# Kernel tuning notes

Measured on AMD Instinct MI355X. Metric: run time of the kernel, lower is better.

## Reference

```python
import jax, jax.numpy as jnp
import numpy as np

B, S, HID, NH = 1, 2048, 2048, 16
HD = HID // NH
HALF = HD // 2
# quantization scales (registered buffers / pack() scales in the original module)
ATTN_IN_SCALE = 0.02   # attn_input_scale: dequant scale of int8 hidden_states
Q_OUT_SCALE = 0.05     # q_output_scale
K_OUT_SCALE = 0.05     # k_output_scale
V_OUT_SCALE = 0.04     # v_output_scale
Q_ROT_SCALE = 0.06     # q_rotary_output_scale
K_ROT_SCALE = 0.06     # k_rotary_output_scale
OUT_IN_SCALE = 0.03    # out_input_scale
W_ALPHA = 0.002        # folded int8 GEMM alpha for q/k/v W8A8B8O8Linear
BETA = 1.0             # bias scale of W8A8B8O8Linear
O_ALPHA = 0.001        # folded alpha for o_proj W8A8BFP32OFP32Linear
PROB_SCALE = 1.0 / 127.0  # attention-prob int8 quant scale
INV_SQRT_HD = float(1.0 / np.sqrt(HD))


def _q8(x):
    # saturating int8 quantization (values kept in float32)
    return jnp.clip(jnp.round(x), -127.0, 127.0)


def setup_inputs() -> dict:
    key = jax.random.key(0)
    ks = jax.random.split(key, 10)
    hidden_states = jax.random.normal(ks[0], (B, S, HID), jnp.float32)
    pos = jnp.arange(S, dtype=jnp.float32)
    inv_freq = 1.0 / (10000.0 ** (jnp.arange(0, HD, 2, dtype=jnp.float32) / HD))
    freqs = pos[:, None] * inv_freq[None, :]          # (S, HD//2)
    cos, sin = jnp.cos(freqs), jnp.sin(freqs)
    w8 = lambda k: jax.random.randint(k, (HID, HID), -127, 128).astype(jnp.float32)
    b8 = lambda k: jax.random.randint(k, (HID,), -127, 128).astype(jnp.float32)
    return dict(
        hidden_states=hidden_states, cos=cos, sin=sin,
        wq=w8(ks[1]), wk=w8(ks[2]), wv=w8(ks[3]), wo=w8(ks[4]),
        bq=b8(ks[5]), bk=b8(ks[6]), bv=b8(ks[7]),
        bo=jax.random.normal(ks[8], (HID,), jnp.float32) * 0.01,
    )


def reference(hidden_states, cos, sin, wq, wk, wv, wo, bq, bk, bv, bo):
    # quantize activations to int8 (done upstream of the module in smoothquant)
    x8 = _q8(hidden_states / ATTN_IN_SCALE)                       # (B,S,HID) int8 vals

    # W8A8B8O8Linear: int8 GEMM, alpha-scaled, int8 bias, saturate to int8
    def lin8(x, w, b):
        return _q8(jnp.einsum('bsi,oi->bso', x, w) * W_ALPHA + BETA * b)

    q8, k8, v8 = lin8(x8, wq, bq), lin8(x8, wk, bk), lin8(x8, wv, bv)

    # int8_rotary_embedding_fwd: dequant -> split-half rotary -> requant
    def rope(x8_flat, in_scale, out_scale):
        x = x8_flat.reshape(B, S, NH, HD) * in_scale
        x0, x1 = x[..., :HALF], x[..., HALF:]
        c, s_ = cos[None, :, None, :], sin[None, :, None, :]
        rot = jnp.concatenate([x0 * c - x1 * s_, x0 * s_ + x1 * c], axis=-1)
        return _q8(rot / out_scale)

    q = rope(q8, Q_OUT_SCALE, Q_ROT_SCALE)                        # (B,S,NH,HD)
    k = rope(k8, K_OUT_SCALE, K_ROT_SCALE)
    v = v8.reshape(B, S, NH, HD)

    # smooth_llama_context_attn_fwd: int8 QK^T -> fp32 scores -> causal softmax
    scores = jnp.einsum('bqhd,bkhd->bhqk', q, k) * (Q_ROT_SCALE * K_ROT_SCALE * INV_SQRT_HD)
    causal = jnp.tril(jnp.ones((S, S), bool))
    scores = jnp.where(causal[None, None], scores, -1e9)
    p = jax.nn.softmax(scores, axis=-1)
    p8 = _q8(p * 127.0)                                           # quantize probs to int8
    # int8 PV bmm, rescale and saturate to int8 for o_proj input
    o8 = _q8(jnp.einsum('bhqk,bkhd->bqhd', p8, v) * (PROB_SCALE * V_OUT_SCALE / OUT_IN_SCALE))
    o8 = o8.reshape(B, S, HID)

    # W8A8BFP32OFP32Linear: int8 GEMM, fp32 alpha + fp32 bias
    out = jnp.einsum('bso,po->bsp', o8, wo) * O_ALPHA + bo
    return out
```

## Files before the change

kernel.cpp:

```cpp
#include <hip/hip_runtime.h>
#include <math.h>

typedef __attribute__((ext_vector_type(4))) int i32x4;
typedef signed char s8;

constexpr int S   = 2048;
constexpr int HID = 2048;
constexpr int NH  = 16;
constexpr int HD  = 128;
constexpr int HALF = 64;

#define SCORE_SCALE ((float)(0.06 * 0.06 * 0.08838834764831845))
#define OSCALE      ((float)(((1.0 / 127.0) * 0.04) / 0.03))

__device__ __forceinline__ float clip127(float r){
  return fminf(fmaxf(r, -127.0f), 127.0f);
}
__device__ __forceinline__ i32x4 mfma_i8(i32x4 a, i32x4 b, i32x4 c){
  return __builtin_amdgcn_mfma_i32_16x16x64_i8(a, b, c, 0, 0, 0);
}
__device__ __forceinline__ void async16(const void* g, void* l){
  __builtin_amdgcn_global_load_lds(
      (const __attribute__((address_space(1))) unsigned*)g,
      (__attribute__((address_space(3))) unsigned*)l, 16, 0, 0);
}
template<int ROWS>
__device__ __forceinline__ void stage_async_swz(s8* dst, const s8* src, int stride){
  const int tid = threadIdx.x;
#pragma unroll
  for (int i = 0; i < ROWS/32; ++i){
    int o = i*256 + tid;
    int row = o >> 3, ch = o & 7;
    async16(src + (size_t)row*stride + ((ch ^ (row & 7))*16), dst + o*16);
  }
}
__device__ __forceinline__ i32x4 rd16(const s8* buf, int row, int ch){
  return *(const i32x4*)(buf + row*128 + ((ch ^ (row & 7))*16));
}
__device__ __forceinline__ int tri_qt(int t){
  int qt = (int)((sqrtf(8.f*t + 1.f) - 1.f)*0.5f);
  while ((qt+1)*(qt+2)/2 <= t) ++qt;
  while (qt*(qt+1)/2 > t) --qt;
  return qt;
}

__global__ void cvt_all(const float* __restrict__ hid, const float* __restrict__ wq,
                        const float* __restrict__ wk, const float* __restrict__ wv,
                        const float* __restrict__ wo, s8* __restrict__ xd,
                        s8* __restrict__ qd, s8* __restrict__ kd,
                        s8* __restrict__ vd, s8* __restrict__ od, int n){
  const float* srcs[5] = {hid, wq, wk, wv, wo};
  s8* dsts[5] = {xd, qd, kd, vd, od};
  int which = blockIdx.y;
  const float* src = srcs[which];
  s8* dst = dsts[which];
  int i = (blockIdx.x * blockDim.x + threadIdx.x) * 4;
  if (i >= n) return;
  float4 v = *(const float4*)(src + i);
  float x[4] = {v.x, v.y, v.z, v.w};
  unsigned packed = 0;
#pragma unroll
  for (int j = 0; j < 4; ++j){
    int b;
    if (which == 0) b = (int)clip127(rintf(x[j] / 0.02f));
    else            b = (int)x[j];
    packed |= ((unsigned)(b & 255)) << (8*j);
  }
  *(unsigned*)(dst + i) = packed;
}

__global__ __launch_bounds__(256)
void gemm_qkv(const s8* __restrict__ A, const s8* __restrict__ W,
              const float* __restrict__ bq, const float* __restrict__ bk,
              const float* __restrict__ bv, s8* __restrict__ Out){
#pragma clang fp contract(off)
  constexpr int Kd = 2048, N = 2048;
  const int z = blockIdx.z;
  const s8* Bt = W + (size_t)z*(4u<<20);
  s8* Y = Out + (size_t)z*(4u<<20);
  const float* bss[3] = {bq, bk, bv};
  const float* bias = bss[z];
  __shared__ __attribute__((aligned(16))) s8 As[128*128];
  __shared__ __attribute__((aligned(16))) s8 Bs[128*128];
  const int lin = blockIdx.x + (blockIdx.y << 4);
  const int virt = (lin & 7)*32 + (lin >> 3);
  const int bm = virt & 15, bn = virt >> 4;
  const int tid = threadIdx.x;
  const int wid = tid >> 6, lane = tid & 63;
  const int wm = wid >> 1, wn = wid & 1;
  const int col16 = lane & 15, g = lane >> 4;
  i32x4 acc[4][4] = {};
  const s8* Ab = A + (size_t)(bm*128)*Kd;
  const s8* Bb = Bt + (size_t)(bn*128)*Kd;
  for (int kt = 0; kt < 16; ++kt){
    stage_async_swz<128>(As, Ab + kt*128, Kd);
    stage_async_swz<128>(Bs, Bb + kt*128, Kd);
    __syncthreads();
#pragma unroll
    for (int kk = 0; kk < 2; ++kk){
      i32x4 af[4], bf[4];
#pragma unroll
      for (int i = 0; i < 4; ++i) af[i] = rd16(As, wm*64 + i*16 + col16, kk*4 + g);
#pragma unroll
      for (int j = 0; j < 4; ++j) bf[j] = rd16(Bs, wn*64 + j*16 + col16, kk*4 + g);
#pragma unroll
      for (int i = 0; i < 4; ++i)
#pragma unroll
        for (int j = 0; j < 4; ++j)
          acc[i][j] = mfma_i8(af[i], bf[j], acc[i][j]);
    }
    __syncthreads();
  }
#pragma unroll
  for (int i = 0; i < 4; ++i){
#pragma unroll
    for (int j = 0; j < 4; ++j){
      int row0 = bm*128 + wm*64 + i*16 + g*4;
      int col  = bn*128 + wn*64 + j*16 + col16;
#pragma unroll
      for (int r = 0; r < 4; ++r){
        float t = (float)acc[i][j][r] * 0.002f;
        t = t + bias[col];
        Y[(size_t)(row0 + r)*N + col] = (s8)(int)clip127(rintf(t));
      }
    }
  }
}

__global__ __launch_bounds__(256)
void gemm_o(const s8* __restrict__ A, const s8* __restrict__ Bt,
            const float* __restrict__ bias, float* __restrict__ Y){
#pragma clang fp contract(off)
  constexpr int Kd = 2048, N = 2048;
  __shared__ __attribute__((aligned(16))) s8 As[128*128];
  __shared__ __attribute__((aligned(16))) s8 Bs[64*128];
  const int lin = blockIdx.x + (blockIdx.y << 4);
  const int virt = (lin & 7)*64 + (lin >> 3);
  const int bm = virt & 15, bn = virt >> 4;
  const int tid = threadIdx.x;
  const int wid = tid >> 6, lane = tid & 63;
  const int wm = wid >> 1, wn = wid & 1;
  const int col16 = lane & 15, g = lane >> 4;
  i32x4 acc[4][2] = {};
  const s8* Ab = A + (size_t)(bm*128)*Kd;
  const s8* Bb = Bt + (size_t)(bn*64)*Kd;
  for (int kt = 0; kt < 16; ++kt){
    stage_async_swz<128>(As, Ab + kt*128, Kd);
    stage_async_swz<64>(Bs, Bb + kt*128, Kd);
    __syncthreads();
#pragma unroll
    for (int kk = 0; kk < 2; ++kk){
      i32x4 af[4], bf[2];
#pragma unroll
      for (int i = 0; i < 4; ++i) af[i] = rd16(As, wm*64 + i*16 + col16, kk*4 + g);
#pragma unroll
      for (int j = 0; j < 2; ++j) bf[j] = rd16(Bs, wn*32 + j*16 + col16, kk*4 + g);
#pragma unroll
      for (int i = 0; i < 4; ++i)
#pragma unroll
        for (int j = 0; j < 2; ++j)
          acc[i][j] = mfma_i8(af[i], bf[j], acc[i][j]);
    }
    __syncthreads();
  }
#pragma unroll
  for (int i = 0; i < 4; ++i){
#pragma unroll
    for (int j = 0; j < 2; ++j){
      int row0 = bm*128 + wm*64 + i*16 + g*4;
      int col  = bn*64 + wn*32 + j*16 + col16;
#pragma unroll
      for (int r = 0; r < 4; ++r){
        float t = (float)acc[i][j][r] * 0.001f;
        t = t + bias[col];
        Y[(size_t)(row0 + r)*N + col] = t;
      }
    }
  }
}

__global__ void rope_qk(s8* __restrict__ q, s8* __restrict__ k,
                        const float* __restrict__ cosp, const float* __restrict__ sinp){
#pragma clang fp contract(off)
  int idx = blockIdx.x * blockDim.x + threadIdx.x;
  int t4 = (idx & 15) * 4;
  int h  = (idx >> 4) & (NH-1);
  int s  = idx >> 8;
  if (s >= S) return;
  float4 c4 = *(const float4*)(cosp + s*HALF + t4);
  float4 s4 = *(const float4*)(sinp + s*HALF + t4);
  float cc[4] = {c4.x, c4.y, c4.z, c4.w}, ss[4] = {s4.x, s4.y, s4.z, s4.w};
  int base = s*HID + h*HD + t4;
  {
    int a0 = *(const int*)(q + base), a1 = *(const int*)(q + base + HALF);
    unsigned o0 = 0, o1 = 0;
#pragma unroll
    for (int j = 0; j < 4; ++j){
      float x0 = (float)((s8)(a0 >> (8*j))) * 0.05f;
      float x1 = (float)((s8)(a1 >> (8*j))) * 0.05f;
      float r0 = x0*cc[j] - x1*ss[j];
      float r1 = x0*ss[j] + x1*cc[j];
      o0 |= ((unsigned)(((int)clip127(rintf(r0 / 0.06f))) & 255)) << (8*j);
      o1 |= ((unsigned)(((int)clip127(rintf(r1 / 0.06f))) & 255)) << (8*j);
    }
    *(unsigned*)(q + base) = o0; *(unsigned*)(q + base + HALF) = o1;
  }
  {
    int a0 = *(const int*)(k + base), a1 = *(const int*)(k + base + HALF);
    unsigned o0 = 0, o1 = 0;
#pragma unroll
    for (int j = 0; j < 4; ++j){
      float x0 = (float)((s8)(a0 >> (8*j))) * 0.05f;
      float x1 = (float)((s8)(a1 >> (8*j))) * 0.05f;
      float r0 = x0*cc[j] - x1*ss[j];
      float r1 = x0*ss[j] + x1*cc[j];
      o0 |= ((unsigned)(((int)clip127(rintf(r0 / 0.06f))) & 255)) << (8*j);
      o1 |= ((unsigned)(((int)clip127(rintf(r1 / 0.06f))) & 255)) << (8*j);
    }
    *(unsigned*)(k + base) = o0; *(unsigned*)(k + base + HALF) = o1;
  }
}

__global__ void vtrans(const s8* __restrict__ v, s8* __restrict__ vt){
  __shared__ __attribute__((aligned(16))) s8 t[128*144];
  int s0 = blockIdx.x * 128, h = blockIdx.y;
  int tid = threadIdx.x;
#pragma unroll
  for (int i = 0; i < 4; ++i){
    int vv = i*256 + tid, r = vv >> 3, ch = vv & 7;
    *(i32x4*)(t + r*144 + ch*16) = *(const i32x4*)(v + (size_t)(s0 + r)*HID + h*HD + ch*16);
  }
  __syncthreads();
#pragma unroll
  for (int i = 0; i < 4; ++i){
    int vv = i*256 + tid, d = vv >> 3, sc = (vv & 7)*16;
    s8 tmp[16];
#pragma unroll
    for (int j = 0; j < 16; ++j) tmp[j] = t[(sc + j)*144 + d];
    *(i32x4*)(vt + (size_t)(h*HD + d)*S + s0 + sc) = *(i32x4*)tmp;
  }
}

__global__ __launch_bounds__(256)
void attn_stats(const s8* __restrict__ qr, const s8* __restrict__ kr,
                float2* __restrict__ stats){
  const int x = blockIdx.x, h = blockIdx.y;
  const int tri = x >> 1, half = x & 1;
  const int qt = tri_qt(tri);
  const int kt = tri - qt*(qt+1)/2;
  const int q0 = qt*128 + half*64;
  const int tid = threadIdx.x, wid = tid >> 6, lane = tid & 63;
  const int col16 = lane & 15, g = lane >> 4;
  __shared__ __attribute__((aligned(16))) s8 Ks[128*128];

  stage_async_swz<128>(Ks, kr + (size_t)(kt*128)*HID + h*HD, HID);
  const s8* qb = qr + (size_t)(q0 + wid*16 + col16)*HID + h*HD + g*16;
  i32x4 aq[2];
  aq[0] = *(const i32x4*)(qb);
  aq[1] = *(const i32x4*)(qb + 64);
  __syncthreads();

  i32x4 sc[8] = {};
#pragma unroll
  for (int kk = 0; kk < 2; ++kk){
#pragma unroll
    for (int j = 0; j < 8; ++j){
      i32x4 bk = rd16(Ks, j*16 + col16, kk*4 + g);
      sc[j] = mfma_i8(aq[kk], bk, sc[j]);
    }
  }

  const bool diag = (kt == qt);
#pragma unroll
  for (int r = 0; r < 4; ++r){
    int rit = half*64 + wid*16 + g*4 + r;
    int qrow = qt*128 + rit;
    int mi = (int)0x80000000;
#pragma unroll
    for (int j = 0; j < 8; ++j){
      int v = sc[j][r];
      if (diag && (kt*128 + j*16 + col16 > qrow)) v = (int)0x80000000;
      mi = max(mi, v);
    }
    mi = max(mi, __shfl_xor(mi, 1));
    mi = max(mi, __shfl_xor(mi, 2));
    mi = max(mi, __shfl_xor(mi, 4));
    mi = max(mi, __shfl_xor(mi, 8));
    float mf = (float)mi * SCORE_SCALE;
    float st = 0.f;
#pragma unroll
    for (int j = 0; j < 8; ++j){
      float arg;
      if (diag && (kt*128 + j*16 + col16 > qrow)) arg = -1e30f;
      else arg = (float)sc[j][r] * SCORE_SCALE - mf;
      st += __expf(arg);
    }
    st += __shfl_xor(st, 1);
    st += __shfl_xor(st, 2);
    st += __shfl_xor(st, 4);
    st += __shfl_xor(st, 8);
    if (col16 == 0) stats[(size_t)(h*136 + tri)*128 + rit] = make_float2(mf, st);
  }
}

__global__ void attn_reduce(const float2* __restrict__ stats, float2* __restrict__ ml){
  const int row = threadIdx.x, qt = blockIdx.x, h = blockIdx.y;
  const int tri = qt*(qt+1)/2;
  float m = -3.0e38f;
  for (int kt = 0; kt <= qt; ++kt)
    m = fmaxf(m, stats[(size_t)(h*136 + tri + kt)*128 + row].x);
  float l = 0.f;
  for (int kt = 0; kt <= qt; ++kt){
    float2 s = stats[(size_t)(h*136 + tri + kt)*128 + row];
    l += s.y * __expf(s.x - m);
  }
  ml[(h*16 + qt)*128 + row] = make_float2(m, l);
}

__global__ __launch_bounds__(256)
void attn_score(const s8* __restrict__ qr, const s8* __restrict__ kr,
                const float2* __restrict__ ml, s8* __restrict__ P8){
  const int x = blockIdx.x, h = blockIdx.y;
  const int tri = x >> 1, half = x & 1;
  const int qt = tri_qt(tri);
  const int kt = tri - qt*(qt+1)/2;
  const int q0 = qt*128 + half*64;
  const int tid = threadIdx.x, wid = tid >> 6, lane = tid & 63;
  const int col16 = lane & 15, g = lane >> 4;
  __shared__ __attribute__((aligned(16))) s8 Ks[128*128];
  __shared__ __attribute__((aligned(16))) s8 Pl[64*128];

  stage_async_swz<128>(Ks, kr + (size_t)(kt*128)*HID + h*HD, HID);
  const s8* qb = qr + (size_t)(q0 + wid*16 + col16)*HID + h*HD + g*16;
  i32x4 aq[2];
  aq[0] = *(const i32x4*)(qb);
  aq[1] = *(const i32x4*)(qb + 64);
  float m[4], c[4];
#pragma unroll
  for (int r = 0; r < 4; ++r){
    float2 t = ml[(h*16 + qt)*128 + half*64 + wid*16 + g*4 + r];
    m[r] = t.x;
    c[r] = 127.0f / t.y;
  }
  __syncthreads();

  const bool diag = (kt == qt);
#pragma unroll
  for (int j = 0; j < 8; ++j){
    i32x4 s0 = {};
    s0 = mfma_i8(aq[0], rd16(Ks, j*16 + col16, g), s0);
    s0 = mfma_i8(aq[1], rd16(Ks, j*16 + col16, 4 + g), s0);
    int colk = j*16 + col16;
#pragma unroll
    for (int r = 0; r < 4; ++r){
      int row = wid*16 + g*4 + r;
      int qrow = q0 + row;
      float p8v = 0.0f;
      if (!diag || (kt*128 + colk) <= qrow){
        float sv = (float)s0[r] * SCORE_SCALE;
        p8v = clip127(rintf(__expf(sv - m[r]) * c[r]));
      }
      Pl[row*128 + colk] = (s8)(int)p8v;
    }
  }
  __syncthreads();
  s8* dst = P8 + (size_t)(h*136 + tri)*16384 + half*8192;
#pragma unroll
  for (int i = 0; i < 2; ++i){
    int o = i*256 + tid;
    *(i32x4*)(dst + o*16) = *(const i32x4*)(Pl + o*16);
  }
}

__global__ __launch_bounds__(256)
void attn_pv(const s8* __restrict__ P8, const s8* __restrict__ vt8,
             s8* __restrict__ o8){
  const int qt = 15 - blockIdx.x;
  const int h = blockIdx.y, dh = blockIdx.z;
  const int tri = qt*(qt+1)/2;
  const int tid = threadIdx.x, wid = tid >> 6, lane = tid & 63;
  const int wm = wid >> 1, wn = wid & 1;
  const int col16 = lane & 15, g = lane >> 4;
  __shared__ __attribute__((aligned(16))) s8 Ps[128*128];
  __shared__ __attribute__((aligned(16))) s8 Vs[64*128];

  i32x4 acc[4][2] = {};
  for (int kt = 0; kt <= qt; ++kt){
    stage_async_swz<128>(Ps, P8 + (size_t)(h*136 + tri + kt)*16384, 128);
    stage_async_swz<64>(Vs, vt8 + (size_t)(h*HD + dh*64)*S + kt*128, S);
    __syncthreads();
#pragma unroll
    for (int kk = 0; kk < 2; ++kk){
      i32x4 af[4], bf[2];
#pragma unroll
      for (int i = 0; i < 4; ++i) af[i] = rd16(Ps, wm*64 + i*16 + col16, kk*4 + g);
#pragma unroll
      for (int j = 0; j < 2; ++j) bf[j] = rd16(Vs, wn*32 + j*16 + col16, kk*4 + g);
#pragma unroll
      for (int i = 0; i < 4; ++i)
#pragma unroll
        for (int j = 0; j < 2; ++j)
          acc[i][j] = mfma_i8(af[i], bf[j], acc[i][j]);
    }
    __syncthreads();
  }
#pragma unroll
  for (int i = 0; i < 4; ++i)
#pragma unroll
    for (int j = 0; j < 2; ++j)
#pragma unroll
      for (int r = 0; r < 4; ++r){
        int row = qt*128 + wm*64 + i*16 + g*4 + r;
        int d = dh*64 + wn*32 + j*16 + col16;
        o8[(size_t)row*HID + h*HD + d] = (s8)(int)clip127(rintf((float)acc[i][j][r] * OSCALE));
      }
}

extern "C" void kernel_launch(void* const* d_in, const int* in_sizes, int n_in,
                              void* d_out, int out_size, void* d_ws, size_t ws_size,
                              hipStream_t stream) {
  const float* hidden = (const float*)d_in[0];
  const float* cosp   = (const float*)d_in[1];
  const float* sinp   = (const float*)d_in[2];
  const float* wq     = (const float*)d_in[3];
  const float* wk     = (const float*)d_in[4];
  const float* wv     = (const float*)d_in[5];
  const float* wo     = (const float*)d_in[6];
  const float* bq     = (const float*)d_in[7];
  const float* bk     = (const float*)d_in[8];
  const float* bv     = (const float*)d_in[9];
  const float* bo     = (const float*)d_in[10];
  float* out = (float*)d_out;

  const size_t MB = 1024*1024;
  s8* ws8 = (s8*)d_ws;
  s8* x8  = ws8 + 0*MB;
  s8* wq8 = ws8 + 4*MB;
  s8* wk8 = ws8 + 8*MB;
  s8* wv8 = ws8 + 12*MB;
  s8* wo8 = ws8 + 16*MB;
  s8* q8  = ws8 + 20*MB;
  s8* k8  = ws8 + 24*MB;
  s8* v8  = ws8 + 28*MB;
  s8* vt8 = ws8 + 32*MB;
  s8* P8  = ws8 + 36*MB;
  s8* o8  = x8;
  float2* stats = (float2*)(ws8 + 4*MB);
  float2* mlb   = (float2*)(ws8 + 4*MB + 2400*1024);

  const int n = HID*HID;
  dim3 b256(256);

  cvt_all<<<dim3(n/1024, 5), b256, 0, stream>>>(hidden, wq, wk, wv, wo,
                                                x8, wq8, wk8, wv8, wo8, n);

  gemm_qkv<<<dim3(16, 16, 3), b256, 0, stream>>>(x8, wq8, bq, bk, bv, q8);

  rope_qk<<<(S*NH*16)/256, b256, 0, stream>>>(q8, k8, cosp, sinp);
  vtrans<<<dim3(S/128, NH), b256, 0, stream>>>(v8, vt8);

  attn_stats<<<dim3(272, 16), b256, 0, stream>>>(q8, k8, stats);
  attn_reduce<<<dim3(16, 16), dim3(128), 0, stream>>>(stats, mlb);
  attn_score<<<dim3(272, 16), b256, 0, stream>>>(q8, k8, mlb, P8);
  attn_pv<<<dim3(16, 16, 2), b256, 0, stream>>>(P8, vt8, o8);

  gemm_o<<<dim3(16, 32), b256, 0, stream>>>(o8, wo8, bo, out);
}
```

Measured before the change: 154.7 us.

## Triple-buffer QKV GEMM LDS tiles with async prefetch two stages ahead

The QKV int8 GEMM now splits K into 64-wide tiles held in a three-slot LDS ring. Each tile's global-to-LDS async loads are issued two iterations ahead, and explicit vmcnt waits plus one barrier per step replace the old load-sync-compute-sync loop. The goal is to hide global memory latency behind MFMA work and drop one barrier per step. In exchange the K step is smaller, so each step does fewer MFMAs per barrier, and correctness depends on the hand-written vmcnt counts matching the outstanding loads.

After: 144.4 us. 1.07x faster.

```diff
diff --git a/kernel.cpp b/kernel.cpp
--- a/kernel.cpp
+++ b/kernel.cpp
@@ -36,6 +36,19 @@
 }
 __device__ __forceinline__ i32x4 rd16(const s8* buf, int row, int ch){
   return *(const i32x4*)(buf + row*128 + ((ch ^ (row & 7))*16));
+}
+__device__ __forceinline__ void stage64(s8* dst, const s8* src, int stride){
+  const int tid = threadIdx.x;
+#pragma unroll
+  for (int i = 0; i < 2; ++i){
+    int o = i*256 + tid;
+    int row = o >> 2, slot = o & 3;
+    int ch = slot ^ ((row >> 2) & 3);
+    async16(src + (size_t)row*stride + ch*16, dst + o*16);
+  }
+}
+__device__ __forceinline__ i32x4 rd64(const s8* buf, int row, int g){
+  return *(const i32x4*)(buf + row*64 + ((g ^ ((row >> 2) & 3))*16));
 }
 __device__ __forceinline__ int tri_qt(int t){
   int qt = (int)((sqrtf(8.f*t + 1.f) - 1.f)*0.5f);
@@ -74,14 +87,14 @@
               const float* __restrict__ bq, const float* __restrict__ bk,
               const float* __restrict__ bv, s8* __restrict__ Out){
 #pragma clang fp contract(off)
-  constexpr int Kd = 2048, N = 2048;
+  constexpr int Kd = 2048, N = 2048, NT = 32;
   const int z = blockIdx.z;
   const s8* Bt = W + (size_t)z*(4u<<20);
   s8* Y = Out + (size_t)z*(4u<<20);
   const float* bss[3] = {bq, bk, bv};
   const float* bias = bss[z];
-  __shared__ __attribute__((aligned(16))) s8 As[128*128];
-  __shared__ __attribute__((aligned(16))) s8 Bs[128*128];
+  __shared__ __attribute__((aligned(16))) s8 As[3][128*64];
+  __shared__ __attribute__((aligned(16))) s8 Bs[3][128*64];
   const int lin = blockIdx.x + (blockIdx.y << 4);
   const int virt = (lin & 7)*32 + (lin >> 3);
   const int bm = virt & 15, bn = virt >> 4;
@@ -92,25 +105,35 @@
   i32x4 acc[4][4] = {};
   const s8* Ab = A + (size_t)(bm*128)*Kd;
   const s8* Bb = Bt + (size_t)(bn*128)*Kd;
-  for (int kt = 0; kt < 16; ++kt){
-    stage_async_swz<128>(As, Ab + kt*128, Kd);
-    stage_async_swz<128>(Bs, Bb + kt*128, Kd);
-    __syncthreads();
-#pragma unroll
-    for (int kk = 0; kk < 2; ++kk){
-      i32x4 af[4], bf[4];
-#pragma unroll
-      for (int i = 0; i < 4; ++i) af[i] = rd16(As, wm*64 + i*16 + col16, kk*4 + g);
-#pragma unroll
-      for (int j = 0; j < 4; ++j) bf[j] = rd16(Bs, wn*64 + j*16 + col16, kk*4 + g);
-#pragma unroll
-      for (int i = 0; i < 4; ++i)
-#pragma unroll
-        for (int j = 0; j < 4; ++j)
-          acc[i][j] = mfma_i8(af[i], bf[j], acc[i][j]);
-    }
-    __syncthreads();
-  }
+
+  stage64(As[0], Ab, Kd);       stage64(Bs[0], Bb, Kd);
+  stage64(As[1], Ab + 64, Kd);  stage64(Bs[1], Bb + 64, Kd);
+  asm volatile("s_waitcnt vmcnt(4)" ::: "memory");
+  __builtin_amdgcn_s_barrier();
+
+  for (int T = 0; T < NT; ++T){
+    const int nxt = T + 2;
+    if (nxt < NT){
+      stage64(As[nxt%3], Ab + nxt*64, Kd);
+      stage64(Bs[nxt%3], Bb + nxt*64, Kd);
+    }
+    const s8* as = As[T%3];
+    const s8* bs = Bs[T%3];
+    i32x4 af[4], bf[4];
+#pragma unroll
+    for (int i = 0; i < 4; ++i) af[i] = rd64(as, wm*64 + i*16 + col16, g);
+#pragma unroll
+    for (int j = 0; j < 4; ++j) bf[j] = rd64(bs, wn*64 + j*16 + col16, g);
+#pragma unroll
+    for (int i = 0; i < 4; ++i)
+#pragma unroll
+      for (int j = 0; j < 4; ++j)
+        acc[i][j] = mfma_i8(af[i], bf[j], acc[i][j]);
+    if (nxt < NT) asm volatile("s_waitcnt vmcnt(4)" ::: "memory");
+    else          asm volatile("s_waitcnt vmcnt(0)" ::: "memory");
+    __builtin_amdgcn_s_barrier();
+  }
+
 #pragma unroll
   for (int i = 0; i < 4; ++i){
 #pragma unroll
```
